# Optimization experiments

Measured on AMD Instinct MI355X. Metric: run time of the kernel, lower is better.

Reference implementation:

```python
import jax, jax.numpy as jnp
import numpy as np

SCALES = (2, 4, 8)  # primitive_scales, one per branch


def setup_inputs() -> dict:
    key = jax.random.key(0)
    k0, k1, k2, k3, k4 = jax.random.split(key, 5)
    B, C, H, W = 16, 256, 128, 128
    s = 1.0 / np.sqrt(C).astype(np.float32)
    return {
        "x": jax.random.normal(k0, (B, C, H, W), jnp.float32),
        "W_proto": jax.random.normal(k1, (3, C, C), jnp.float32) * s,
        "W_frame": jax.random.normal(k2, (3, C, C), jnp.float32) * s,
        "W_out": jax.random.normal(k3, (3, C, C), jnp.float32) * s,
        "W_fuse": jax.random.normal(k4, (C, 3 * C), jnp.float32) * (1.0 / np.sqrt(3 * C).astype(np.float32)),
    }


def _branch(x, Wp, Wf, Wo, P):
    # x: [B,C,H,W]; adaptive_avg_pool2d(x, (H, P)) with W % P == 0 == mean over equal bins along W
    B, C, H, W = x.shape
    proto = x.reshape(B, C, H, P, W // P).mean(axis=-1)        # [B,C,H,P]
    proto = jnp.einsum('oc,bchp->bohp', Wp, proto)             # proto_proj (1x1 conv)
    q = jnp.einsum('oc,bchw->bhwo', Wf, x)                     # frame_proj + permute -> [B,H,W,C]
    # att = q @ k, k = proto.permute(0,2,1,3) -> [B,H,C,P]
    att = jnp.einsum('bhwc,bchp->bhwp', q, proto) * (1.0 / jnp.sqrt(jnp.float32(C)))
    att = jax.nn.softmax(att, axis=-1)                         # [B,H,W,P]
    # v = proto.permute(0,2,3,1) -> [B,H,P,C]; msg = att @ v -> [B,H,W,C]
    msg = jnp.einsum('bhwp,bchp->bhwc', att, proto)
    return jnp.einsum('oc,bhwc->bohw', Wo, msg)                # out_proj -> [B,C,H,W]


def reference(x, W_proto, W_frame, W_out, W_fuse):
    outs = [_branch(x, W_proto[i], W_frame[i], W_out[i], SCALES[i]) for i in range(len(SCALES))]
    cat = jnp.concatenate(outs, axis=1)                        # [B, 3C, H, W]
    return jnp.einsum('oc,bchw->bohw', W_fuse, cat) + x
```

## Files before the change

kernel.cpp:

```cpp
#include <hip/hip_runtime.h>
#include <hip/hip_bf16.h>
#include <math.h>
#include <stdint.h>

#define CC   256
#define HW   (128*128)
#define MAT  (CC*CC)
#define NBH  2048
#define N0   4096
#define N1   8192
#define N2   16384

typedef __attribute__((ext_vector_type(8))) short bf16x8;
typedef __attribute__((ext_vector_type(4))) float f32x4;
typedef __attribute__((address_space(3))) uint32_t lds_u32_t;
typedef __attribute__((address_space(1))) const uint32_t glb_u32_t;

__global__ __launch_bounds__(256) void k_mats1(
    const float* __restrict__ Wp, const float* __restrict__ Wf,
    const float* __restrict__ Wo, const float* __restrict__ Wfu,
    __hip_bfloat16* __restrict__ A, float* __restrict__ E)
{
    int idx = blockIdx.x;
    int t = threadIdx.x;
    if (idx < 3*CC) {
        int i = idx >> 8, c = idx & 255;
        const float* wf = Wf + (size_t)i*MAT;
        const float* wp = Wp + (size_t)i*MAT;
        float acc = 0.f;
        for (int o = 0; o < CC; ++o)
            acc += wf[o*CC + c] * wp[o*CC + t];
        A[(size_t)i*512*CC + (size_t)c*CC + t] = __float2bfloat16(acc);
    } else {
        idx -= 3*CC;
        int i = idx >> 8, o = idx & 255;
        const float* wo = Wo + (size_t)i*MAT;
        const float* wfu = Wfu + (size_t)o*(3*CC) + i*CC;
        float acc = 0.f;
        for (int c3 = 0; c3 < CC; ++c3)
            acc += wfu[c3] * wo[c3*CC + t];
        E[(size_t)i*MAT + (size_t)o*CC + t] = acc;
    }
}

__global__ __launch_bounds__(256) void k_mats2(
    const float* __restrict__ Wp, const float* __restrict__ E,
    __hip_bfloat16* __restrict__ A)
{
    int idx = blockIdx.x;
    int i = idx >> 8, o = idx & 255;
    int t = threadIdx.x;
    const float* e = E + (size_t)i*MAT + (size_t)o*CC;
    const float* wp = Wp + (size_t)i*MAT;
    float acc = 0.f;
    for (int c = 0; c < CC; ++c)
        acc += e[c] * wp[c*CC + t];
    A[(size_t)i*512*CC + (size_t)(256+o)*CC + t] = __float2bfloat16(acc);
}

__global__ __launch_bounds__(256, 4) void k_poolA(
    const float* __restrict__ x, float* __restrict__ binsG)
{
    int bc = blockIdx.x;
    int t = threadIdx.x;
    const float4* xp = (const float4*)(x + (size_t)bc*HW) + t;
    __shared__ float bins[128][9];
    float4 v[16];
    #pragma unroll
    for (int i = 0; i < 16; ++i) v[i] = xp[i*256];
    int hb = t >> 5, bin = (t & 31) >> 2;
    #pragma unroll
    for (int i = 0; i < 16; ++i) {
        float s = v[i].x + v[i].y + v[i].z + v[i].w;
        s += __shfl_xor(s, 1);
        s += __shfl_xor(s, 2);
        if ((t & 3) == 0) bins[i*8 + hb][bin] = s;
    }
    __syncthreads();
    int h = t >> 1, b0 = (t & 1) * 4;
    float4 o;
    o.x = bins[h][b0+0]; o.y = bins[h][b0+1];
    o.z = bins[h][b0+2]; o.w = bins[h][b0+3];
    ((float4*)binsG)[(size_t)bc*256 + t] = o;
}

__global__ __launch_bounds__(256) void k_poolB(
    const float* __restrict__ binsG, __hip_bfloat16* __restrict__ Bt)
{
    int bh = blockIdx.x;
    int b = bh >> 7, h = bh & 127;
    int c = threadIdx.x;
    const float* g = binsG + (((size_t)b*256 + c)*128 + h)*8;
    float4 lo = *(const float4*)(g);
    float4 hi = *(const float4*)(g + 4);
    float b8[8] = {lo.x, lo.y, lo.z, lo.w, hi.x, hi.y, hi.z, hi.w};

    __hip_bfloat16* B0 = Bt;
    __hip_bfloat16* B1 = Bt + (size_t)N0*CC;
    __hip_bfloat16* B2 = Bt + (size_t)(N0+N1)*CC;
    B0[((size_t)bh*2 + 0)*CC + c] = __float2bfloat16((b8[0]+b8[1]+b8[2]+b8[3]) * (1.f/64.f));
    B0[((size_t)bh*2 + 1)*CC + c] = __float2bfloat16((b8[4]+b8[5]+b8[6]+b8[7]) * (1.f/64.f));
    #pragma unroll
    for (int j = 0; j < 4; ++j)
        B1[((size_t)bh*4 + j)*CC + c] = __float2bfloat16((b8[2*j]+b8[2*j+1]) * (1.f/32.f));
    #pragma unroll
    for (int j = 0; j < 8; ++j)
        B2[((size_t)bh*8 + j)*CC + c] = __float2bfloat16(b8[j] * (1.f/16.f));
}

__global__ __launch_bounds__(128) void k_gemm(
    const __hip_bfloat16* __restrict__ A,
    const __hip_bfloat16* __restrict__ Bt,
    __hip_bfloat16* __restrict__ Cc)
{
    int blk = blockIdx.x;
    int br, lb, LP, poff;
    if (blk < 256)      { br = 0; lb = blk;       LP = 1; poff = 0; }
    else if (blk < 768) { br = 1; lb = blk - 256; LP = 2; poff = 2; }
    else                { br = 2; lb = blk - 768; LP = 3; poff = 6; }
    size_t aoff  = (size_t)br*512*CC;
    size_t btoff = (br == 0) ? 0 : (br == 1 ? (size_t)N0*CC : (size_t)(N0+N1)*CC);
    const __hip_bfloat16* Ab = A  + aoff;
    const __hip_bfloat16* Bb = Bt + btoff;

    int rb = lb & 3, cb = lb >> 2;
    int wv = threadIdx.x >> 6, lane = threadIdx.x & 63;
    int row0 = rb*128 + wv*64;
    int col0 = cb*64;
    int lr = lane & 15, lk = (lane >> 4) * 8;

    f32x4 acc[4][4] = {};
    for (int kk = 0; kk < CC; kk += 32) {
        bf16x8 af[4], bfr[4];
        #pragma unroll
        for (int m = 0; m < 4; ++m)
            af[m] = *reinterpret_cast<const bf16x8*>(Ab + (size_t)(row0 + m*16 + lr)*CC + kk + lk);
        #pragma unroll
        for (int n = 0; n < 4; ++n)
            bfr[n] = *reinterpret_cast<const bf16x8*>(Bb + (size_t)(col0 + n*16 + lr)*CC + kk + lk);
        #pragma unroll
        for (int m = 0; m < 4; ++m)
            #pragma unroll
            for (int n = 0; n < 4; ++n)
                acc[m][n] = __builtin_amdgcn_mfma_f32_16x16x32_bf16(af[m], bfr[n], acc[m][n], 0, 0, 0);
    }

    int cr = (lane >> 4) * 4, ccol = lane & 15;
    int pm = (1 << LP) - 1;
    #pragma unroll
    for (int m = 0; m < 4; ++m) {
        #pragma unroll
        for (int n = 0; n < 4; ++n) {
            int colg = col0 + n*16 + ccol;
            int bh = colg >> LP, p = colg & pm;
            __hip_bfloat16* dst = Cc + (size_t)bh*8192 + poff + p;
            #pragma unroll
            for (int j = 0; j < 4; ++j) {
                int r = row0 + m*16 + cr + j;
                dst[r*16] = __float2bfloat16(acc[m][n][j]);
            }
        }
    }
}

template<int L>
__device__ __forceinline__ void softmax2(float2* a) {
    float mx = a[0].x, my = a[0].y;
    #pragma unroll
    for (int j = 1; j < L; ++j) { mx = fmaxf(mx, a[j].x); my = fmaxf(my, a[j].y); }
    float sx = 0.f, sy = 0.f;
    #pragma unroll
    for (int j = 0; j < L; ++j) {
        a[j].x = __expf(a[j].x - mx); sx += a[j].x;
        a[j].y = __expf(a[j].y - my); sy += a[j].y;
    }
    float rx = 1.f / sx, ry = 1.f / sy;
    #pragma unroll
    for (int j = 0; j < L; ++j) { a[j].x *= rx; a[j].y *= ry; }
}

__global__ __launch_bounds__(512, 1) void k_main(
    const float* __restrict__ x, const __hip_bfloat16* __restrict__ Cc,
    float* __restrict__ out)
{
    int bh = blockIdx.x;
    int b = bh >> 7, h = bh & 127;
    int t = threadIdx.x;
    int lane = t & 63;
    int wv = __builtin_amdgcn_readfirstlane(t >> 6);
    const uint32_t* Cb = (const uint32_t*)(Cc + (size_t)bh*8192);
    const float* xg = x + ((size_t)b*CC)*HW + h*128;
    float2* o2 = (float2*)out + ((size_t)b*CC)*(HW/2) + h*64 + lane;

    __shared__ float  xlds[256][128];
    __shared__ float2 red[4][64][15];

    float2 att[14];
    #pragma unroll
    for (int p = 0; p < 14; ++p) att[p] = make_float2(0.f, 0.f);

    const float* gsrc = xg + (size_t)(lane >> 5)*HW + (lane & 31)*4;

    #pragma unroll
    for (int j = 0; j < 16; ++j) {
        int c0 = wv*32 + 2*j;
        __builtin_amdgcn_global_load_lds(
            (glb_u32_t*)(gsrc + (size_t)c0*HW),
            (lds_u32_t*)&xlds[c0][0], 16, 0, 0);
    }
    __builtin_amdgcn_sched_barrier(0);

    #define CONSA(J, VM)                                                    \
        asm volatile("s_waitcnt vmcnt(" #VM ")" ::: "memory");              \
        __builtin_amdgcn_sched_barrier(0);                                  \
        {                                                                   \
            const int c0 = wv*32 + 2*(J);                                   \
            const uint32_t* wr0 = Cb + (size_t)c0*8;                        \
            float2 x0 = *(const float2*)&xlds[c0][lane*2];                  \
            float2 x1 = *(const float2*)&xlds[c0+1][lane*2];                \
            _Pragma("unroll")                                               \
            for (int p = 0; p < 7; ++p) {                                   \
                uint32_t u0 = wr0[p], u1 = wr0[8+p];                        \
                float a0 = __uint_as_float(u0 << 16);                       \
                float b0 = __uint_as_float(u0 & 0xFFFF0000u);               \
                float a1 = __uint_as_float(u1 << 16);                       \
                float b1 = __uint_as_float(u1 & 0xFFFF0000u);               \
                att[2*p].x   += x0.x*a0 + x1.x*a1;                          \
                att[2*p].y   += x0.y*a0 + x1.y*a1;                          \
                att[2*p+1].x += x0.x*b0 + x1.x*b1;                          \
                att[2*p+1].y += x0.y*b0 + x1.y*b1;                          \
            }                                                               \
        }

    CONSA(0, 15); CONSA(1, 14); CONSA(2, 13); CONSA(3, 12);
    CONSA(4, 11); CONSA(5, 10); CONSA(6,  9); CONSA(7,  8);
    CONSA(8,  7); CONSA(9,  6); CONSA(10, 5); CONSA(11, 4);
    CONSA(12, 3); CONSA(13, 2); CONSA(14, 1); CONSA(15, 0);
    #undef CONSA

    if (wv >= 4) {
        #pragma unroll
        for (int p = 0; p < 14; ++p) red[wv-4][lane][p] = att[p];
    }
    __syncthreads();
    if (wv < 4) {
        #pragma unroll
        for (int p = 0; p < 14; ++p) {
            float2 r = red[wv][lane][p];
            att[p].x += r.x; att[p].y += r.y;
        }
    }
    __syncthreads();
    if (wv >= 1 && wv < 4) {
        #pragma unroll
        for (int p = 0; p < 14; ++p) red[wv][lane][p] = att[p];
    }
    __syncthreads();
    if (wv == 0) {
        #pragma unroll
        for (int p = 0; p < 14; ++p) {
            float2 r1 = red[1][lane][p], r2 = red[2][lane][p], r3 = red[3][lane][p];
            att[p].x = (att[p].x + r1.x + r2.x + r3.x) * 0.0625f;
            att[p].y = (att[p].y + r1.y + r2.y + r3.y) * 0.0625f;
        }
        softmax2<2>(att + 0);
        softmax2<4>(att + 2);
        softmax2<8>(att + 6);
        #pragma unroll
        for (int p = 0; p < 14; ++p) red[0][lane][p] = att[p];
    }
    __syncthreads();
    #pragma unroll
    for (int p = 0; p < 14; ++p) att[p] = red[0][lane][p];

    #pragma unroll 8
    for (int jj = 0; jj < 32; ++jj) {
        int ch = wv*32 + jj;
        const uint32_t* wr = Cb + (size_t)(256 + ch)*8;
        float2 xv = *(const float2*)&xlds[ch][lane*2];
        float2 acc = xv;
        #pragma unroll
        for (int p = 0; p < 7; ++p) {
            uint32_t u = wr[p];
            float vlo = __uint_as_float(u << 16);
            float vhi = __uint_as_float(u & 0xFFFF0000u);
            acc.x += att[2*p].x * vlo + att[2*p+1].x * vhi;
            acc.y += att[2*p].y * vlo + att[2*p+1].y * vhi;
        }
        o2[(size_t)ch * (HW/2)] = acc;
    }
}

extern "C" void kernel_launch(void* const* d_in, const int* in_sizes, int n_in,
                              void* d_out, int out_size, void* d_ws, size_t ws_size,
                              hipStream_t stream)
{
    (void)in_sizes; (void)n_in; (void)out_size; (void)ws_size;
    const float* x   = (const float*)d_in[0];
    const float* Wp  = (const float*)d_in[1];
    const float* Wf  = (const float*)d_in[2];
    const float* Wo  = (const float*)d_in[3];
    const float* Wfu = (const float*)d_in[4];
    float* out = (float*)d_out;

    char* wsb = (char*)d_ws;
    float*          E     = (float*)wsb;
    __hip_bfloat16* A     = (__hip_bfloat16*)(wsb + 786432);
    __hip_bfloat16* Bt    = (__hip_bfloat16*)(wsb + 1572864);
    __hip_bfloat16* Cc    = (__hip_bfloat16*)(wsb + 16252928);
    float*          binsG = (float*)(wsb + 16252928);

    k_mats1<<<dim3(6*CC),  dim3(256), 0, stream>>>(Wp, Wf, Wo, Wfu, A, E);
    k_mats2<<<dim3(3*CC),  dim3(256), 0, stream>>>(Wp, E, A);
    k_poolA<<<dim3(4096),  dim3(256), 0, stream>>>(x, binsG);
    k_poolB<<<dim3(NBH),   dim3(256), 0, stream>>>(binsG, Bt);
    k_gemm <<<dim3(1792),  dim3(128), 0, stream>>>(A, Bt, Cc);
    k_main <<<dim3(NBH),   dim3(512), 0, stream>>>(x, Cc, out);
}
```

Measured before the change: 390.7 us.

## Fuse pooling with bf16 transpose of x and shrink main kernel traffic

The pooling kernel now also writes a bf16 copy of x transposed to [B,H,C,W]. The main kernel then streams contiguous bf16 rows instead of strided fp32 channels, and runs at 256 threads with two blocks per CU and a shorter cross-wave reduction. The aim is to cut global read traffic in the main kernel and raise occupancy. The cost is an extra bf16 write and read of x, and the residual add now uses bf16-rounded x, which may hurt accuracy.

```diff
diff --git a/kernel.cpp b/kernel.cpp
--- a/kernel.cpp
+++ b/kernel.cpp
@@ -58,30 +58,68 @@
     A[(size_t)i*512*CC + (size_t)(256+o)*CC + t] = __float2bfloat16(acc);
 }
 
-__global__ __launch_bounds__(256, 4) void k_poolA(
-    const float* __restrict__ x, float* __restrict__ binsG)
-{
-    int bc = blockIdx.x;
+__global__ __launch_bounds__(256, 4) void k_trans(
+    const float* __restrict__ x, __hip_bfloat16* __restrict__ xT,
+    float* __restrict__ binsG)
+{
+    int blk = blockIdx.x;
+    int b  = blk >> 7;
+    int ct = (blk >> 3) & 15;
+    int ht = blk & 7;
+    int c0 = ct*16, h0 = ht*16;
     int t = threadIdx.x;
-    const float4* xp = (const float4*)(x + (size_t)bc*HW) + t;
-    __shared__ float bins[128][9];
-    float4 v[16];
-    #pragma unroll
-    for (int i = 0; i < 16; ++i) v[i] = xp[i*256];
-    int hb = t >> 5, bin = (t & 31) >> 2;
-    #pragma unroll
-    for (int i = 0; i < 16; ++i) {
-        float s = v[i].x + v[i].y + v[i].z + v[i].w;
-        s += __shfl_xor(s, 1);
-        s += __shfl_xor(s, 2);
-        if ((t & 3) == 0) bins[i*8 + hb][bin] = s;
+
+    __shared__ ushort xt[16*16*128];
+    __shared__ float  bl[16*128];
+
+    #pragma unroll 1
+    for (int batch = 0; batch < 2; ++batch) {
+        float4 v[16];
+        #pragma unroll
+        for (int k = 0; k < 16; ++k) {
+            int kk = batch*16 + k;
+            int i = kk >> 1, j8 = (kk & 1)*8;
+            const float4* src = (const float4*)x +
+                ((size_t)(b*256 + c0 + i)*128 + h0 + j8)*32 + t;
+            v[k] = *src;
+        }
+        #pragma unroll
+        for (int k = 0; k < 16; ++k) {
+            int kk = batch*16 + k;
+            int i = kk >> 1;
+            int j = (kk & 1)*8 + (t >> 5);
+            int w4 = t & 31;
+            float s = v[k].x + v[k].y + v[k].z + v[k].w;
+            s += __shfl_xor(s, 1);
+            s += __shfl_xor(s, 2);
+            if ((w4 & 3) == 0) bl[i*128 + j*8 + (w4 >> 2)] = s;
+            union { __hip_bfloat16 h[4]; ushort4 q; } cu;
+            cu.h[0] = __float2bfloat16(v[k].x);
+            cu.h[1] = __float2bfloat16(v[k].y);
+            cu.h[2] = __float2bfloat16(v[k].z);
+            cu.h[3] = __float2bfloat16(v[k].w);
+            *(ushort4*)&xt[((i*16 + j)*128 + w4*4)] = cu.q;
+        }
     }
     __syncthreads();
-    int h = t >> 1, b0 = (t & 1) * 4;
-    float4 o;
-    o.x = bins[h][b0+0]; o.y = bins[h][b0+1];
-    o.z = bins[h][b0+2]; o.w = bins[h][b0+3];
-    ((float4*)binsG)[(size_t)bc*256 + t] = o;
+
+    #pragma unroll 4
+    for (int j = 0; j < 16; ++j) {
+        size_t base4 = (((size_t)(b*128 + h0 + j)*256 + c0)*128) >> 2;
+        #pragma unroll
+        for (int p = 0; p < 2; ++p) {
+            int q = p*256 + t;
+            int i = q >> 5, w4 = q & 31;
+            ushort4 val = *(const ushort4*)&xt[(i*16 + j)*128 + w4*4];
+            ((ushort4*)xT)[base4 + q] = val;
+        }
+    }
+    #pragma unroll
+    for (int it = 0; it < 8; ++it) {
+        int q = it*256 + t;
+        int c = q >> 7, rem = q & 127;
+        binsG[((size_t)(b*256 + c0 + c)*128 + h0)*8 + rem] = bl[c*128 + rem];
+    }
 }
 
 __global__ __launch_bounds__(256) void k_poolB(
@@ -179,8 +217,8 @@
     for (int j = 0; j < L; ++j) { a[j].x *= rx; a[j].y *= ry; }
 }
 
-__global__ __launch_bounds__(512, 1) void k_main(
-    const float* __restrict__ x, const __hip_bfloat16* __restrict__ Cc,
+__global__ __launch_bounds__(256, 2) void k_main(
+    const __hip_bfloat16* __restrict__ xT, const __hip_bfloat16* __restrict__ Cc,
     float* __restrict__ out)
 {
     int bh = blockIdx.x;
@@ -189,79 +227,79 @@
     int lane = t & 63;
     int wv = __builtin_amdgcn_readfirstlane(t >> 6);
     const uint32_t* Cb = (const uint32_t*)(Cc + (size_t)bh*8192);
-    const float* xg = x + ((size_t)b*CC)*HW + h*128;
-    float2* o2 = (float2*)out + ((size_t)b*CC)*(HW/2) + h*64 + lane;
-
-    __shared__ float  xlds[256][128];
-    __shared__ float2 red[4][64][15];
+    const __hip_bfloat16* xrow = xT + (size_t)bh*256*128;
+    float2* o2 = (float2*)out + (size_t)b*256*8192 + h*64 + lane;
+
+    __shared__ __hip_bfloat16 xlds[256*128];
+    __shared__ float2 red[2][64][15];
+
+    const __hip_bfloat16* gsrc = xrow + wv*64*128 + lane*8;
+    #pragma unroll
+    for (int d = 0; d < 16; ++d) {
+        __builtin_amdgcn_global_load_lds(
+            (glb_u32_t*)(gsrc + d*4*128),
+            (lds_u32_t*)&xlds[(wv*64 + d*4)*128], 16, 0, 0);
+    }
+    __builtin_amdgcn_sched_barrier(0);
 
     float2 att[14];
     #pragma unroll
     for (int p = 0; p < 14; ++p) att[p] = make_float2(0.f, 0.f);
-
-    const float* gsrc = xg + (size_t)(lane >> 5)*HW + (lane & 31)*4;
-
-    #pragma unroll
-    for (int j = 0; j < 16; ++j) {
-        int c0 = wv*32 + 2*j;
-        __builtin_amdgcn_global_load_lds(
-            (glb_u32_t*)(gsrc + (size_t)c0*HW),
-            (lds_u32_t*)&xlds[c0][0], 16, 0, 0);
-    }
-    __builtin_amdgcn_sched_barrier(0);
-
-    #define CONSA(J, VM)                                                    \
+    const uint32_t* xl32 = (const uint32_t*)xlds;
+
+    #define CONSA(D, VM)                                                    \
         asm volatile("s_waitcnt vmcnt(" #VM ")" ::: "memory");              \
         __builtin_amdgcn_sched_barrier(0);                                  \
         {                                                                   \
-            const int c0 = wv*32 + 2*(J);                                   \
-            const uint32_t* wr0 = Cb + (size_t)c0*8;                        \
-            float2 x0 = *(const float2*)&xlds[c0][lane*2];                  \
-            float2 x1 = *(const float2*)&xlds[c0+1][lane*2];                \
+            const int cb0 = wv*64 + (D)*4;                                  \
             _Pragma("unroll")                                               \
-            for (int p = 0; p < 7; ++p) {                                   \
-                uint32_t u0 = wr0[p], u1 = wr0[8+p];                        \
-                float a0 = __uint_as_float(u0 << 16);                       \
-                float b0 = __uint_as_float(u0 & 0xFFFF0000u);               \
-                float a1 = __uint_as_float(u1 << 16);                       \
-                float b1 = __uint_as_float(u1 & 0xFFFF0000u);               \
-                att[2*p].x   += x0.x*a0 + x1.x*a1;                          \
-                att[2*p].y   += x0.y*a0 + x1.y*a1;                          \
-                att[2*p+1].x += x0.x*b0 + x1.x*b1;                          \
-                att[2*p+1].y += x0.y*b0 + x1.y*b1;                          \
+            for (int q = 0; q < 4; ++q) {                                   \
+                int c = cb0 + q;                                            \
+                const uint32_t* wr = Cb + (size_t)c*8;                      \
+                uint32_t xu = xl32[c*64 + lane];                            \
+                float2 xv;                                                  \
+                xv.x = __uint_as_float(xu << 16);                           \
+                xv.y = __uint_as_float(xu & 0xFFFF0000u);                   \
+                _Pragma("unroll")                                           \
+                for (int p = 0; p < 7; ++p) {                               \
+                    uint32_t u = wr[p];                                     \
+                    float mlo = __uint_as_float(u << 16);                   \
+                    float mhi = __uint_as_float(u & 0xFFFF0000u);           \
+                    att[2*p].x   += xv.x * mlo;  att[2*p].y   += xv.y * mlo; \
+                    att[2*p+1].x += xv.x * mhi;  att[2*p+1].y += xv.y * mhi; \
+                }                                                           \
             }                                                               \
         }
 
-    CONSA(0, 15); CONSA(1, 14); CONSA(2, 13); CONSA(3, 12);
-    CONSA(4, 11); CONSA(5, 10); CONSA(6,  9); CONSA(7,  8);
-    CONSA(8,  7); CONSA(9,  6); CONSA(10, 5); CONSA(11, 4);
-    CONSA(12, 3); CONSA(13, 2); CONSA(14, 1); CONSA(15, 0);
+    CONSA(0, 15) CONSA(1, 14) CONSA(2, 13) CONSA(3, 12)
+    CONSA(4, 11) CONSA(5, 10) CONSA(6,  9) CONSA(7,  8)
+    CONSA(8,  7) CONSA(9,  6) CONSA(10, 5) CONSA(11, 4)
+    CONSA(12, 3) CONSA(13, 2) CONSA(14, 1) CONSA(15, 0)
     #undef CONSA
 
-    if (wv >= 4) {
-        #pragma unroll
-        for (int p = 0; p < 14; ++p) red[wv-4][lane][p] = att[p];
+    if (wv >= 2) {
+        #pragma unroll
+        for (int p = 0; p < 14; ++p) red[wv-2][lane][p] = att[p];
     }
     __syncthreads();
-    if (wv < 4) {
+    if (wv < 2) {
         #pragma unroll
         for (int p = 0; p < 14; ++p) {
             float2 r = red[wv][lane][p];
             att[p].x += r.x; att[p].y += r.y;
         }
-    }
-    __syncthreads();
-    if (wv >= 1 && wv < 4) {
-        #pragma unroll
-        for (int p = 0; p < 14; ++p) red[wv][lane][p] = att[p];
+        if (wv == 1) {
+            #pragma unroll
+            for (int p = 0; p < 14; ++p) red[1][lane][p] = att[p];
+        }
     }
     __syncthreads();
     if (wv == 0) {
         #pragma unroll
         for (int p = 0; p < 14; ++p) {
-            float2 r1 = red[1][lane][p], r2 = red[2][lane][p], r3 = red[3][lane][p];
-            att[p].x = (att[p].x + r1.x + r2.x + r3.x) * 0.0625f;
-            att[p].y = (att[p].y + r1.y + r2.y + r3.y) * 0.0625f;
+            float2 r = red[1][lane][p];
+            att[p].x = (att[p].x + r.x) * 0.0625f;
+            att[p].y = (att[p].y + r.y) * 0.0625f;
         }
         softmax2<2>(att + 0);
         softmax2<4>(att + 2);
@@ -273,12 +311,14 @@
     #pragma unroll
     for (int p = 0; p < 14; ++p) att[p] = red[0][lane][p];
 
-    #pragma unroll 8
-    for (int jj = 0; jj < 32; ++jj) {
-        int ch = wv*32 + jj;
-        const uint32_t* wr = Cb + (size_t)(256 + ch)*8;
-        float2 xv = *(const float2*)&xlds[ch][lane*2];
-        float2 acc = xv;
+    #pragma unroll 4
+    for (int jj = 0; jj < 64; ++jj) {
+        int c = wv*64 + jj;
+        const uint32_t* wr = Cb + (size_t)(256 + c)*8;
+        uint32_t xu = xl32[c*64 + lane];
+        float2 acc;
+        acc.x = __uint_as_float(xu << 16);
+        acc.y = __uint_as_float(xu & 0xFFFF0000u);
         #pragma unroll
         for (int p = 0; p < 7; ++p) {
             uint32_t u = wr[p];
@@ -287,7 +327,7 @@
             acc.x += att[2*p].x * vlo + att[2*p+1].x * vhi;
             acc.y += att[2*p].y * vlo + att[2*p+1].y * vhi;
         }
-        o2[(size_t)ch * (HW/2)] = acc;
+        o2[(size_t)c*8192] = acc;
     }
 }
 
@@ -309,11 +349,12 @@
     __hip_bfloat16* Bt    = (__hip_bfloat16*)(wsb + 1572864);
     __hip_bfloat16* Cc    = (__hip_bfloat16*)(wsb + 16252928);
     float*          binsG = (float*)(wsb + 16252928);
-
-    k_mats1<<<dim3(6*CC),  dim3(256), 0, stream>>>(Wp, Wf, Wo, Wfu, A, E);
-    k_mats2<<<dim3(3*CC),  dim3(256), 0, stream>>>(Wp, E, A);
-    k_poolA<<<dim3(4096),  dim3(256), 0, stream>>>(x, binsG);
-    k_poolB<<<dim3(NBH),   dim3(256), 0, stream>>>(binsG, Bt);
-    k_gemm <<<dim3(1792),  dim3(128), 0, stream>>>(A, Bt, Cc);
-    k_main <<<dim3(NBH),   dim3(512), 0, stream>>>(x, Cc, out);
-}
+    __hip_bfloat16* xT    = (__hip_bfloat16*)(wsb + 49807360);
+
+    k_mats1<<<dim3(6*CC), dim3(256), 0, stream>>>(Wp, Wf, Wo, Wfu, A, E);
+    k_mats2<<<dim3(3*CC), dim3(256), 0, stream>>>(Wp, E, A);
+    k_trans<<<dim3(2048), dim3(256), 0, stream>>>(x, xT, binsG);
+    k_poolB<<<dim3(NBH),  dim3(256), 0, stream>>>(binsG, Bt);
+    k_gemm <<<dim3(1792), dim3(128), 0, stream>>>(A, Bt, Cc);
+    k_main <<<dim3(NBH),  dim3(256), 0, stream>>>(xT, Cc, out);
+}
```

New measurement: 368.5 us. 5.7% less time.
